# Kernel optimization log

Measured on AMD Instinct MI355X. Metric: run time of the kernel, lower is better.

The kernel has to match this reference:

```python
import jax, jax.numpy as jnp
import numpy as np

B, N, INC, H, W = 1, 6, 256, 56, 100
DD, CC = 41, 64                         # depth bins (4..45 step 1), cam feat channels
NX, NY, NZ = 33, 33, 2                  # BEV grid from pc_range=[-50,-50,-5,50,50,3], grid=3
CZ = CC * NZ                            # 128 channels into bevencode
DXV = jnp.array([3.0, 3.0, 3.0], jnp.float32)
BXV = jnp.array([-48.5, -48.5, -3.5], jnp.float32)


def _frustum():
    ds = jnp.arange(4.0, 45.0, 1.0)                      # (41,)
    xs = jnp.linspace(0.0, 1599.0, W)
    ys = jnp.linspace(0.0, 899.0, H)
    d = jnp.broadcast_to(ds[:, None, None], (DD, H, W))
    xg = jnp.broadcast_to(xs[None, None, :], (DD, H, W))
    yg = jnp.broadcast_to(ys[None, :, None], (DD, H, W))
    return jnp.stack([xg, yg, d], -1)                    # (D,H,W,3)


def _conv(x, w):
    return jax.lax.conv_general_dilated(x, w, (1, 1), 'SAME',
                                        dimension_numbers=('NCHW', 'OIHW', 'NCHW'))


def _bn_relu(x, s, b, m, v):
    inv = s / jnp.sqrt(v + 1e-5)
    return jax.nn.relu(x * inv[None, :, None, None] + (b - m * inv)[None, :, None, None])


def _forward(x, rots, trans, dn_w, dn_b,
             bw1, bn1_s, bn1_b, bn1_m, bn1_v,
             bw2, bn2_s, bn2_b, bn2_m, bn2_v,
             bw3, bn3_s, bn3_b, bn3_m, bn3_v,
             bw4, bn4_s, bn4_b, bn4_m, bn4_v):
    # ---- CamEncode: 1x1 depthnet -> softmax depth dist + context features ----
    xf = x.reshape(B * N, INC, H, W)
    y = _conv(xf, dn_w) + dn_b[None, :, None, None]
    depth = jax.nn.softmax(y[:, :DD], axis=1).reshape(B, N, DD, H, W)
    feat = y[:, DD:DD + CC].reshape(B, N, CC, H, W)
    # ---- get_geometry: (u*d, v*d, d) -> ego frame ----
    fr = _frustum()                                                     # (D,H,W,3)
    pts = jnp.concatenate([fr[..., :2] * fr[..., 2:3], fr[..., 2:3]], -1)
    geom = jnp.einsum('bnij,dhwj->bndhwi', rots, pts) + trans[:, :, None, None, None, :]
    # ---- voxel indices (torch .long() truncates toward zero) ----
    coor = ((geom - (BXV - DXV / 2.0)) / DXV).astype(jnp.int32)         # (B,N,D,H,W,3)
    cx, cy, cz = coor[..., 0], coor[..., 1], coor[..., 2]
    kept = (cx >= 0) & (cx < NX) & (cy >= 0) & (cy < NY) & (cz >= 0) & (cz < NZ)
    bidx = jnp.arange(B, dtype=jnp.int32)[:, None, None, None, None]
    ranks = ((bidx * NZ + cz) * NY + cy) * NX + cx                      # bev rank per point
    nvox = B * NZ * NY * NX
    seg = jnp.where(kept, ranks, nvox).reshape(-1)                      # drop bucket = nvox
    # ---- lift: depth-weighted outer product, splat: segment-sum by voxel ----
    vol = depth[..., None] * feat.transpose(0, 1, 3, 4, 2)[:, :, None]  # (B,N,D,H,W,C)
    bev = jax.ops.segment_sum(vol.reshape(-1, CC), seg, num_segments=nvox + 1)[:nvox]
    bev = bev.reshape(B, NZ, NY, NX, CC).transpose(0, 4, 1, 2, 3).reshape(B, CZ, NY, NX)
    h = _bn_relu(_conv(bev, bw1), bn1_s, bn1_b, bn1_m, bn1_v)
    h = _bn_relu(_conv(h, bw2), bn2_s, bn2_b, bn2_m, bn2_v)
    h = _bn_relu(_conv(h, bw3), bn3_s, bn3_b, bn3_m, bn3_v)
    h = _bn_relu(_conv(h, bw4), bn4_s, bn4_b, bn4_m, bn4_v)
    return h                                                            # (B,256,33,33)


def setup_inputs() -> dict:
    key = jax.random.key(0)
    ks = jax.random.split(key, 16)
    x = jax.random.normal(ks[0], (B, N, INC, H, W), jnp.float32)
    # rots = small rotation perturbation composed with intrinsics inverse
    kinv = jnp.array([[1.0 / 800.0, 0.0, -1.0], [0.0, 1.0 / 800.0, -0.5625], [0.0, 0.0, 1.0]], jnp.float32)
    R = jnp.eye(3, dtype=jnp.float32) + 0.05 * jax.random.normal(ks[1], (B, N, 3, 3), jnp.float32)
    rots = jnp.einsum('bnij,jk->bnik', R, kinv)
    trans = 2.0 * jax.random.normal(ks[2], (B, N, 3), jnp.float32)

    def w(k, o, i, kh, kw):
        return jax.random.normal(k, (o, i, kh, kw), jnp.float32) * (2.0 / (i * kh * kw)) ** 0.5

    def bn(k, c):
        k1, k2, k3, k4 = jax.random.split(k, 4)
        return (1.0 + 0.1 * jax.random.normal(k1, (c,), jnp.float32),
                0.1 * jax.random.normal(k2, (c,), jnp.float32),
                0.1 * jax.random.normal(k3, (c,), jnp.float32),
                jax.random.uniform(k4, (c,), jnp.float32, 0.5, 1.5))
    bn1 = bn(ks[7], CZ); bn2 = bn(ks[8], 512); bn3 = bn(ks[9], 512); bn4 = bn(ks[10], 256)
    return dict(
        x=x, rots=rots, trans=trans,
        dn_w=w(ks[3], DD + CC, INC, 1, 1), dn_b=jnp.zeros((DD + CC,), jnp.float32),
        bw1=w(ks[4], CZ, CZ, 3, 3),
        bn1_s=bn1[0], bn1_b=bn1[1], bn1_m=bn1[2], bn1_v=bn1[3],
        bw2=w(ks[5], 512, CZ, 3, 3),
        bn2_s=bn2[0], bn2_b=bn2[1], bn2_m=bn2[2], bn2_v=bn2[3],
        bw3=w(ks[6], 512, 512, 3, 3),
        bn3_s=bn3[0], bn3_b=bn3[1], bn3_m=bn3[2], bn3_v=bn3[3],
        bw4=w(ks[11], 256, 512, 3, 3),
        bn4_s=bn4[0], bn4_b=bn4[1], bn4_m=bn4[2], bn4_v=bn4[3])


def reference(x, rots, trans, dn_w, dn_b,
              bw1, bn1_s, bn1_b, bn1_m, bn1_v,
              bw2, bn2_s, bn2_b, bn2_m, bn2_v,
              bw3, bn3_s, bn3_b, bn3_m, bn3_v,
              bw4, bn4_s, bn4_b, bn4_m, bn4_v):
    return _forward(x, rots, trans, dn_w, dn_b,
                    bw1, bn1_s, bn1_b, bn1_m, bn1_v,
                    bw2, bn2_s, bn2_b, bn2_m, bn2_v,
                    bw3, bn3_s, bn3_b, bn3_m, bn3_v,
                    bw4, bn4_s, bn4_b, bn4_m, bn4_v)
```

## Files before the change

### kernel.cpp

```cpp
#include <hip/hip_runtime.h>
#include <math.h>

#define NCAM  6
#define INC   256
#define HH    56
#define WW    100
#define HW    5600
#define NPIX  33600
#define DDEP  41
#define CFEAT 64
#define NCH   105
#define NXG   33
#define NYG   33
#define NZG   2
#define NVOX  2178
#define PADW  35
#define PADHW 1225
#define NPIXO 1089

typedef short bf16x8 __attribute__((ext_vector_type(8)));
typedef float f32x4  __attribute__((ext_vector_type(4)));

#define Y_OFF    0
#define Y_SZ     (NCAM * NCH * HW)
#define WDH_OFF  (Y_OFF + Y_SZ)
#define WDL_OFF  (WDH_OFF + 16384)
#define W1H_OFF  (WDL_OFF + 16384)
#define W1L_OFF  (W1H_OFF + 73728)
#define W2H_OFF  (W1L_OFF + 73728)
#define W2L_OFF  (W2H_OFF + 294912)
#define W3H_OFF  (W2L_OFF + 294912)
#define W3L_OFF  (W3H_OFF + 1179648)
#define W4H_OFF  (W3L_OFF + 1179648)
#define W4L_OFF  (W4H_OFF + 589824)
#define BEV_OFF  (W4L_OFF + 589824)
#define BEV_SZ   (NVOX * CFEAT)
#define A1_OFF   (BEV_OFF + BEV_SZ)
#define A2_OFF   (A1_OFF + 313600)
#define A3_OFF   (A2_OFF + 313600)
#define P_OFF    (A3_OFF + 313600)
#define P_SZ     4460544
#define WS_END   (P_OFF + P_SZ)

#define BEV_N4   (BEV_SZ / 4)

__device__ __forceinline__ unsigned short f2bf_rn(float f) {
    unsigned u = __builtin_bit_cast(unsigned, f);
    unsigned r = (u + 0x7FFFu + ((u >> 16) & 1u)) >> 16;
    return (unsigned short)r;
}
__device__ __forceinline__ void split_bf(float f, unsigned short& h, unsigned short& l) {
    h = f2bf_rn(f);
    float hf = __builtin_bit_cast(float, (unsigned)h << 16);
    l = f2bf_rn(f - hf);
}
__device__ __forceinline__ void split_bf_trunc(float f, short& h, short& l) {
    unsigned u = __builtin_bit_cast(unsigned, f);
    h = (short)(u >> 16);
    float hf = __builtin_bit_cast(float, u & 0xFFFF0000u);
    float r = f - hf;
    l = (short)(__builtin_bit_cast(unsigned, r) >> 16);
}

template<int COUT, int CIN>
__device__ __forceinline__ void wprep_conv_t(const float* __restrict__ wgt,
                                             unsigned short* __restrict__ wh,
                                             unsigned short* __restrict__ wl,
                                             int i)
{
    constexpr int NCHK = CIN >> 5;
    constexpr int NCOG = COUT >> 4;
    int jj = i & 7, lane = (i >> 3) & 63;
    int r  = i >> 9;
    int chk = r % NCHK; r /= NCHK;
    int cog = r % NCOG; int dydx = r / NCOG;
    int co = cog * 16 + (lane & 15);
    int ci = chk * 32 + (lane >> 4) * 8 + jj;
    float w = wgt[((size_t)co * CIN + ci) * 9 + dydx];
    unsigned short h, l; split_bf(w, h, l);
    wh[i] = h; wl[i] = l;
}

__global__ __launch_bounds__(256) void k_prep(const float* __restrict__ dnw,
                                              const float* __restrict__ bw1,
                                              const float* __restrict__ bw2,
                                              const float* __restrict__ bw3,
                                              const float* __restrict__ bw4,
                                              unsigned short* __restrict__ wdh,
                                              unsigned short* __restrict__ wdl,
                                              unsigned short* __restrict__ w1h,
                                              unsigned short* __restrict__ w1l,
                                              unsigned short* __restrict__ w2h,
                                              unsigned short* __restrict__ w2l,
                                              unsigned short* __restrict__ w3h,
                                              unsigned short* __restrict__ w3l,
                                              unsigned short* __restrict__ w4h,
                                              unsigned short* __restrict__ w4l,
                                              uint4* __restrict__ bev4)
{
    int i = blockIdx.x * 256 + threadIdx.x;
    if (i < BEV_N4) { bev4[i] = make_uint4(0u, 0u, 0u, 0u); return; }
    i -= BEV_N4;
    if (i < 32768) {
        int jj = i & 7, lane = (i >> 3) & 63, chk = (i >> 9) & 7, ct = i >> 12;
        int co = ct * 16 + (lane & 15);
        int ci = chk * 32 + (lane >> 4) * 8 + jj;
        float w = (co < NCH) ? dnw[co * 256 + ci] : 0.f;
        unsigned short h, l; split_bf(w, h, l);
        wdh[i] = h; wdl[i] = l;
        return;
    }
    i -= 32768;
    if (i < 147456)  { wprep_conv_t<128, 128>(bw1, w1h, w1l, i); return; }
    i -= 147456;
    if (i < 589824)  { wprep_conv_t<512, 128>(bw2, w2h, w2l, i); return; }
    i -= 589824;
    if (i < 2359296) { wprep_conv_t<512, 512>(bw3, w3h, w3l, i); return; }
    i -= 2359296;
    if (i < 1179648) { wprep_conv_t<256, 512>(bw4, w4h, w4l, i); return; }
}
#define PREP_TOTAL (BEV_N4 + 32768 + 147456 + 589824 + 2359296 + 1179648)

__global__ __launch_bounds__(256) void k_depthnet_fused(const float* __restrict__ x,
                                                        const unsigned short* __restrict__ wdh,
                                                        const unsigned short* __restrict__ wdl,
                                                        const float* __restrict__ dnb,
                                                        float* __restrict__ y)
{
    const int t  = threadIdx.x;
    const int w  = t >> 6;
    const int l  = t & 63;
    const int lp = l & 15;
    const int q  = l >> 4;
    const int n   = blockIdx.y;
    const int ct0 = blockIdx.z * 4;
    const int px  = blockIdx.x * 64 + w * 16 + lp;
    const bool pok = px < HW;
    const float* xl = x + (size_t)n * INC * HW + (pok ? px : 0);

    f32x4 acc[4];
#pragma unroll
    for (int ct = 0; ct < 4; ++ct) acc[ct] = (f32x4){0.f, 0.f, 0.f, 0.f};

#pragma unroll 2
    for (int ci0 = 0; ci0 < INC; ci0 += 32) {
        float bv[8];
#pragma unroll
        for (int jj = 0; jj < 8; ++jj)
            bv[jj] = xl[(size_t)(ci0 + q * 8 + jj) * HW];
        bf16x8 Bh, Bl;
#pragma unroll
        for (int jj = 0; jj < 8; ++jj) {
            short h, lo; split_bf_trunc(pok ? bv[jj] : 0.f, h, lo);
            Bh[jj] = h; Bl[jj] = lo;
        }
#pragma unroll
        for (int ct = 0; ct < 4; ++ct) {
            const size_t ab = (size_t)(((ct0 + ct) * 8 + (ci0 >> 5)) * 64 + l) * 8;
            bf16x8 Ah = *(const bf16x8*)&wdh[ab];
            bf16x8 Al = *(const bf16x8*)&wdl[ab];
            acc[ct] = __builtin_amdgcn_mfma_f32_16x16x32_bf16(Ah, Bh, acc[ct], 0, 0, 0);
            acc[ct] = __builtin_amdgcn_mfma_f32_16x16x32_bf16(Ah, Bl, acc[ct], 0, 0, 0);
            acc[ct] = __builtin_amdgcn_mfma_f32_16x16x32_bf16(Al, Bh, acc[ct], 0, 0, 0);
        }
    }

    float v[4][4];
#pragma unroll
    for (int ct = 0; ct < 4; ++ct)
#pragma unroll
        for (int j = 0; j < 4; ++j) {
            int co = (ct0 + ct) * 16 + q * 4 + j;
            v[ct][j] = acc[ct][j] + ((co < NCH) ? dnb[co] : 0.f);
        }

    if (ct0 == 0) {
        float m = -3.4e38f;
#pragma unroll
        for (int ct = 0; ct < 4; ++ct)
#pragma unroll
            for (int j = 0; j < 4; ++j) {
                int co = ct * 16 + q * 4 + j;
                if (co < DDEP) m = fmaxf(m, v[ct][j]);
            }
        m = fmaxf(m, __shfl_xor(m, 16));
        m = fmaxf(m, __shfl_xor(m, 32));
        float e[4][4];
        float s = 0.f;
#pragma unroll
        for (int ct = 0; ct < 4; ++ct)
#pragma unroll
            for (int j = 0; j < 4; ++j) {
                int co = ct * 16 + q * 4 + j;
                e[ct][j] = (co < DDEP) ? expf(v[ct][j] - m) : 0.f;
                s += e[ct][j];
            }
        s += __shfl_xor(s, 16);
        s += __shfl_xor(s, 32);
#pragma unroll
        for (int ct = 0; ct < 4; ++ct)
#pragma unroll
            for (int j = 0; j < 4; ++j) {
                int co = ct * 16 + q * 4 + j;
                if (co < DDEP) v[ct][j] = e[ct][j] / s;
            }
    }

    if (pok) {
#pragma unroll
        for (int ct = 0; ct < 4; ++ct)
#pragma unroll
            for (int j = 0; j < 4; ++j) {
                int co = (ct0 + ct) * 16 + q * 4 + j;
                if (co < NCH)
                    y[((size_t)n * NCH + co) * HW + px] = v[ct][j];
            }
    }
}

__global__ __launch_bounds__(256) void k_splat2(const float* __restrict__ y,
                                                const float* __restrict__ rots,
                                                const float* __restrict__ trans,
                                                float* __restrict__ bev)
{
    __shared__ int vox[32 * DDEP];
    const int t  = threadIdx.x;
    const int p0 = blockIdx.x * 32;

    for (int k = t; k < 32 * DDEP; k += 256) {
        int pl = k / DDEP, d = k - pl * DDEP;
        int p = p0 + pl;
        int vx = -1;
        {
            int n = p / HW, hw = p - n * HW;
            int wi = hw % WW, hi = hw / WW;
            const float su = 1599.0f / 99.0f;
            const float sv = 899.0f / 55.0f;
            float u = __fmul_rn((float)wi, su);
            float v = __fmul_rn((float)hi, sv);
            const float* r = rots + n * 9;
            const float* tr = trans + n * 3;
            float dd  = 4.0f + (float)d;
            float pxv = __fmul_rn(u, dd);
            float pyv = __fmul_rn(v, dd);
            float gx = __fadd_rn(__fadd_rn(__fadd_rn(__fmul_rn(r[0], pxv), __fmul_rn(r[1], pyv)), __fmul_rn(r[2], dd)), tr[0]);
            float gy = __fadd_rn(__fadd_rn(__fadd_rn(__fmul_rn(r[3], pxv), __fmul_rn(r[4], pyv)), __fmul_rn(r[5], dd)), tr[1]);
            float gz = __fadd_rn(__fadd_rn(__fadd_rn(__fmul_rn(r[6], pxv), __fmul_rn(r[7], pyv)), __fmul_rn(r[8], dd)), tr[2]);
            int cx = (int)__fdiv_rn(__fadd_rn(gx, 50.0f), 3.0f);
            int cy = (int)__fdiv_rn(__fadd_rn(gy, 50.0f), 3.0f);
            int cz = (int)__fdiv_rn(__fadd_rn(gz, 5.0f), 3.0f);
            if (cx >= 0 && cx < NXG && cy >= 0 && cy < NYG && cz >= 0 && cz < NZG)
                vx = (cz * NYG + cy) * NXG + cx;
        }
        vox[k] = vx;
    }
    __syncthreads();

    const int g  = t >> 5;
    const int pl = t & 31;
    const int p  = p0 + pl;
    int n = p / HW, hw = p - n * HW;
    const float* dbase = y + (size_t)n * NCH * HW + hw;
    const float* fbase = dbase + (size_t)DDEP * HW;
    float f[8];
#pragma unroll
    for (int j = 0; j < 8; ++j) f[j] = fbase[(size_t)(g * 8 + j) * HW];

    float a[8];
#pragma unroll
    for (int j = 0; j < 8; ++j) a[j] = 0.f;
    int cur = -1;
    for (int d = 0; d < DDEP; ++d) {
        int vx = vox[pl * DDEP + d];
        if (vx != cur) {
            if (cur >= 0) {
                float* vp = bev + (size_t)cur * CFEAT + g * 8;
#pragma unroll
                for (int j = 0; j < 8; ++j) atomicAdd(vp + j, a[j]);
            }
            cur = vx;
#pragma unroll
            for (int j = 0; j < 8; ++j) a[j] = 0.f;
        }
        if (vx >= 0) {
            float dval = dbase[(size_t)d * HW];
#pragma unroll
            for (int j = 0; j < 8; ++j) a[j] += __fmul_rn(dval, f[j]);
        }
    }
    if (cur >= 0) {
        float* vp = bev + (size_t)cur * CFEAT + g * 8;
#pragma unroll
        for (int j = 0; j < 8; ++j) atomicAdd(vp + j, a[j]);
    }
}

template<int CIN, int COUT, int SL, int BEVIN>
__global__ __launch_bounds__(256) void k_conv_mfma(const void* __restrict__ actv,
                                                   const unsigned short* __restrict__ wh,
                                                   const unsigned short* __restrict__ wl,
                                                   float* __restrict__ P)
{
    constexpr int CI_PER = CIN / SL;
    constexpr int CHUNKS = CI_PER / 32;
    constexpr int NSLOT  = CHUNKS * 4;
    constexpr int SMASK  = NSLOT - 1;
    constexpr int ROW    = NSLOT * 8;
    constexpr int NCOB = COUT / 64;
    constexpr int G    = NCOB * SL;
    constexpr int GX   = G / 8;
    constexpr int POSN = 140;
    __shared__ unsigned short bs[POSN * ROW];
    const unsigned short* act = (const unsigned short*)actv;
    const float* bevf = (const float*)actv;
    const int t  = threadIdx.x;
    const int w  = t >> 6;
    const int l  = t & 63;
    const int lp = l & 15;
    const int q  = l >> 4;

    const int bid   = blockIdx.x;
    const int xcd   = bid & 7;
    const int slot  = bid >> 3;
    const int ytile = slot % 17;
    const int gon   = slot / 17;
    const int group = xcd * GX + gon;
    const int cobi  = group % NCOB;
    const int sl    = group / NCOB;

    const int y0  = ytile * 2;
    const int cob = cobi * 64 + w * 16;
    const int ci_base = sl * CI_PER;

    int  pos0[5];
    bool vld[5];
#pragma unroll
    for (int ct = 0; ct < 5; ++ct) {
        int tp = ct * 16 + lp;
        int r = tp / 33, c = tp - r * 33;
        bool v = (tp < 66) && (y0 + r < 33);
        vld[ct]  = v;
        pos0[ct] = v ? (r * 35 + c) : 0;
    }

    for (int i = t; i < POSN * NSLOT; i += 256) {
        int pos = i / NSLOT, s = i - pos * NSLOT;
        int gpos = y0 * 35 + pos;
        int sp = s ^ (pos & SMASK);
        uint4 val = make_uint4(0u, 0u, 0u, 0u);
        if (gpos < PADHW) {
            if constexpr (BEVIN) {
                int gy = gpos / 35, gx = gpos - gy * 35;
                if (gy >= 1 && gy <= 33 && gx >= 1 && gx <= 33) {
                    int vx = (gy - 1) * 33 + (gx - 1);
                    int c0 = (ci_base + s * 8) >> 1;
                    float4 v0 = *(const float4*)&bevf[(size_t)vx * 64 + c0];
                    float4 v1 = *(const float4*)&bevf[(size_t)(NPIXO + vx) * 64 + c0];
                    unsigned short o[8] = { f2bf_rn(v0.x), f2bf_rn(v1.x),
                                            f2bf_rn(v0.y), f2bf_rn(v1.y),
                                            f2bf_rn(v0.z), f2bf_rn(v1.z),
                                            f2bf_rn(v0.w), f2bf_rn(v1.w) };
                    val = *(const uint4*)o;
                }
            } else {
                val = *(const uint4*)&act[(size_t)gpos * CIN + ci_base + s * 8];
            }
        }
        *(uint4*)&bs[pos * ROW + sp * 8] = val;
    }
    __syncthreads();

    f32x4 acc[5];
#pragma unroll
    for (int ct = 0; ct < 5; ++ct) acc[ct] = (f32x4){0.f, 0.f, 0.f, 0.f};

#pragma unroll 3
    for (int dydx = 0; dydx < 9; ++dydx) {
        int dy = dydx / 3, dx = dydx - dy * 3;
        int off = dy * 35 + dx;
        bf16x8 Ah[CHUNKS], Al[CHUNKS];
#pragma unroll
        for (int c = 0; c < CHUNKS; ++c) {
            const size_t abase = (size_t)(((dydx * (COUT >> 4) + (cob >> 4)) * (CIN >> 5)
                                           + (ci_base >> 5) + c) * 64 + l) * 8;
            Ah[c] = *(const bf16x8*)&wh[abase];
            Al[c] = *(const bf16x8*)&wl[abase];
        }
#pragma unroll
        for (int ct = 0; ct < 5; ++ct) {
            int pos = pos0[ct] + off;
#pragma unroll
            for (int c = 0; c < CHUNKS; ++c) {
                int sph = (c * 4 + q) ^ (pos & SMASK);
                bf16x8 B = *(const bf16x8*)&bs[pos * ROW + sph * 8];
                acc[ct] = __builtin_amdgcn_mfma_f32_16x16x32_bf16(Ah[c], B, acc[ct], 0, 0, 0);
                acc[ct] = __builtin_amdgcn_mfma_f32_16x16x32_bf16(Al[c], B, acc[ct], 0, 0, 0);
            }
        }
    }

#pragma unroll
    for (int ct = 0; ct < 5; ++ct) {
        if (!vld[ct]) continue;
        int gp = y0 * 33 + ct * 16 + lp;
        float* dst = P + ((size_t)sl * NPIXO + gp) * COUT + cob + q * 4;
        *(f32x4*)dst = acc[ct];
    }
}

template<int SL, int COUT, int FINAL>
__global__ __launch_bounds__(256) void k_finish(const float* __restrict__ P,
                                                const float* __restrict__ bns,
                                                const float* __restrict__ bnb,
                                                const float* __restrict__ bnm,
                                                const float* __restrict__ bnv,
                                                unsigned short* __restrict__ oact,
                                                float* __restrict__ outf)
{
    int i = blockIdx.x * 256 + threadIdx.x;
    constexpr int NP = FINAL ? NPIXO : PADHW;
    if (i >= COUT * NP) return;
    int co = i % COUT, pos = i / COUT;
    if constexpr (FINAL) {
        float s = 0.f;
#pragma unroll
        for (int sl = 0; sl < SL; ++sl)
            s += P[((size_t)sl * NPIXO + pos) * COUT + co];
        float sc = bns[co] / sqrtf(bnv[co] + 1e-5f);
        float bi = bnb[co] - bnm[co] * sc;
        outf[(size_t)co * NPIXO + pos] = fmaxf(fmaf(s, sc, bi), 0.f);
    } else {
        int py = pos / 35, px2 = pos - py * 35;
        bool inz = (py >= 1) && (py <= 33) && (px2 >= 1) && (px2 <= 33);
        unsigned short ov = 0;
        if (inz) {
            int p = (py - 1) * 33 + (px2 - 1);
            float s = 0.f;
#pragma unroll
            for (int sl = 0; sl < SL; ++sl)
                s += P[((size_t)sl * NPIXO + p) * COUT + co];
            float sc = bns[co] / sqrtf(bnv[co] + 1e-5f);
            float bi = bnb[co] - bnm[co] * sc;
            ov = f2bf_rn(fmaxf(fmaf(s, sc, bi), 0.f));
        }
        oact[(size_t)pos * COUT + co] = ov;
    }
}

extern "C" void kernel_launch(void* const* d_in, const int* in_sizes, int n_in,
                              void* d_out, int out_size, void* d_ws, size_t ws_size,
                              hipStream_t stream)
{
    const float* x     = (const float*)d_in[0];
    const float* rots  = (const float*)d_in[1];
    const float* trans = (const float*)d_in[2];
    const float* dnw   = (const float*)d_in[3];
    const float* dnb   = (const float*)d_in[4];
    const float* bw1   = (const float*)d_in[5];
    const float* bn1s  = (const float*)d_in[6];
    const float* bn1b  = (const float*)d_in[7];
    const float* bn1m  = (const float*)d_in[8];
    const float* bn1v  = (const float*)d_in[9];
    const float* bw2   = (const float*)d_in[10];
    const float* bn2s  = (const float*)d_in[11];
    const float* bn2b  = (const float*)d_in[12];
    const float* bn2m  = (const float*)d_in[13];
    const float* bn2v  = (const float*)d_in[14];
    const float* bw3   = (const float*)d_in[15];
    const float* bn3s  = (const float*)d_in[16];
    const float* bn3b  = (const float*)d_in[17];
    const float* bn3m  = (const float*)d_in[18];
    const float* bn3v  = (const float*)d_in[19];
    const float* bw4   = (const float*)d_in[20];
    const float* bn4s  = (const float*)d_in[21];
    const float* bn4b  = (const float*)d_in[22];
    const float* bn4m  = (const float*)d_in[23];
    const float* bn4v  = (const float*)d_in[24];

    float* ws  = (float*)d_ws;
    float* y   = ws + Y_OFF;
    float* bev = ws + BEV_OFF;
    float* P   = ws + P_OFF;
    unsigned short* wdh = (unsigned short*)(ws + WDH_OFF);
    unsigned short* wdl = (unsigned short*)(ws + WDL_OFF);
    unsigned short* w1h = (unsigned short*)(ws + W1H_OFF);
    unsigned short* w1l = (unsigned short*)(ws + W1L_OFF);
    unsigned short* w2h = (unsigned short*)(ws + W2H_OFF);
    unsigned short* w2l = (unsigned short*)(ws + W2L_OFF);
    unsigned short* w3h = (unsigned short*)(ws + W3H_OFF);
    unsigned short* w3l = (unsigned short*)(ws + W3L_OFF);
    unsigned short* w4h = (unsigned short*)(ws + W4H_OFF);
    unsigned short* w4l = (unsigned short*)(ws + W4L_OFF);
    unsigned short* a1  = (unsigned short*)(ws + A1_OFF);
    unsigned short* a2  = (unsigned short*)(ws + A2_OFF);
    unsigned short* a3  = (unsigned short*)(ws + A3_OFF);
    float* out = (float*)d_out;

    k_prep<<<(PREP_TOTAL + 255) / 256, 256, 0, stream>>>(dnw, bw1, bw2, bw3, bw4,
                                                         wdh, wdl, w1h, w1l, w2h, w2l,
                                                         w3h, w3l, w4h, w4l, (uint4*)bev);
    k_depthnet_fused<<<dim3(88, 6, 2), 256, 0, stream>>>(x, wdh, wdl, dnb, y);
    k_splat2<<<1050, 256, 0, stream>>>(y, rots, trans, bev);

    k_conv_mfma<128, 128, 4, 1><<<136, 256, 0, stream>>>(bev, w1h, w1l, P);
    k_finish<4, 128, 0><<<(128 * PADHW + 255) / 256, 256, 0, stream>>>(P, bn1s, bn1b, bn1m, bn1v, a1, nullptr);
    k_conv_mfma<128, 512, 4, 0><<<544, 256, 0, stream>>>(a1, w2h, w2l, P);
    k_finish<4, 512, 0><<<(512 * PADHW + 255) / 256, 256, 0, stream>>>(P, bn2s, bn2b, bn2m, bn2v, a2, nullptr);
    k_conv_mfma<512, 512, 4, 0><<<544, 256, 0, stream>>>(a2, w3h, w3l, P);
    k_finish<4, 512, 0><<<(512 * PADHW + 255) / 256, 256, 0, stream>>>(P, bn3s, bn3b, bn3m, bn3v, a3, nullptr);
    k_conv_mfma<512, 256, 8, 0><<<544, 256, 0, stream>>>(a3, w4h, w4l, P);
    k_finish<8, 256, 1><<<(256 * NPIXO + 255) / 256, 256, 0, stream>>>(P, bn4s, bn4b, bn4m, bn4v, nullptr, out);
}
```

Before: 120.5 us.

## Fuse split-K reduction and BN+ReLU into next conv's input staging

Removes the three intermediate k_finish kernels. Each following conv now reads the previous layer's split-K partial sums directly while staging its input, sums them, applies the BN scale/bias and ReLU, and rounds to bf16 in the load path. Two ping-pong partial buffers replace the single P buffer and the bf16 activation buffers. This saves three launches and one write/read round trip of the activations. In exchange, each conv block re-reads fp32 partials, four slices per element, and halo rows are re-reduced by neighbouring tiles, so input global traffic per conv goes up.

```diff
diff --git a/kernel.cpp b/kernel.cpp
--- a/kernel.cpp
+++ b/kernel.cpp
@@ -35,12 +35,10 @@
 #define W4L_OFF  (W4H_OFF + 589824)
 #define BEV_OFF  (W4L_OFF + 589824)
 #define BEV_SZ   (NVOX * CFEAT)
-#define A1_OFF   (BEV_OFF + BEV_SZ)
-#define A2_OFF   (A1_OFF + 313600)
-#define A3_OFF   (A2_OFF + 313600)
-#define P_OFF    (A3_OFF + 313600)
-#define P_SZ     4460544
-#define WS_END   (P_OFF + P_SZ)
+#define PA_OFF   (BEV_OFF + BEV_SZ)
+#define PBUF_SZ  2230272
+#define PB_OFF   (PA_OFF + PBUF_SZ)
+#define WS_END   (PB_OFF + PBUF_SZ)
 
 #define BEV_N4   (BEV_SZ / 4)
 
@@ -295,8 +293,12 @@
     }
 }
 
-template<int CIN, int COUT, int SL, int BEVIN>
-__global__ __launch_bounds__(256) void k_conv_mfma(const void* __restrict__ actv,
+template<int CIN, int COUT, int SL, int SLP, int MODE>
+__global__ __launch_bounds__(256) void k_conv_mfma(const void* __restrict__ inv,
+                                                   const float* __restrict__ bns,
+                                                   const float* __restrict__ bnb,
+                                                   const float* __restrict__ bnm,
+                                                   const float* __restrict__ bnv,
                                                    const unsigned short* __restrict__ wh,
                                                    const unsigned short* __restrict__ wl,
                                                    float* __restrict__ P)
@@ -311,8 +313,9 @@
     constexpr int GX   = G / 8;
     constexpr int POSN = 140;
     __shared__ unsigned short bs[POSN * ROW];
-    const unsigned short* act = (const unsigned short*)actv;
-    const float* bevf = (const float*)actv;
+    __shared__ float scb[MODE == 0 ? CI_PER * 2 : 2];
+    const float* Pin  = (const float*)inv;
+    const float* bevf = (const float*)inv;
     const int t  = threadIdx.x;
     const int w  = t >> 6;
     const int l  = t & 63;
@@ -343,27 +346,56 @@
         pos0[ct] = v ? (r * 35 + c) : 0;
     }
 
+    if constexpr (MODE == 0) {
+        for (int c = t; c < CI_PER; c += 256) {
+            int ci = ci_base + c;
+            float sc = bns[ci] / sqrtf(bnv[ci] + 1e-5f);
+            scb[c * 2]     = sc;
+            scb[c * 2 + 1] = bnb[ci] - bnm[ci] * sc;
+        }
+        __syncthreads();
+    }
+
     for (int i = t; i < POSN * NSLOT; i += 256) {
         int pos = i / NSLOT, s = i - pos * NSLOT;
         int gpos = y0 * 35 + pos;
         int sp = s ^ (pos & SMASK);
         uint4 val = make_uint4(0u, 0u, 0u, 0u);
         if (gpos < PADHW) {
-            if constexpr (BEVIN) {
-                int gy = gpos / 35, gx = gpos - gy * 35;
-                if (gy >= 1 && gy <= 33 && gx >= 1 && gx <= 33) {
-                    int vx = (gy - 1) * 33 + (gx - 1);
+            int gy = gpos / 35, gx = gpos - gy * 35;
+            bool inz = (gy >= 1) && (gy <= 33) && (gx >= 1) && (gx <= 33);
+            if (inz) {
+                int p = (gy - 1) * 33 + (gx - 1);
+                if constexpr (MODE == 1) {
                     int c0 = (ci_base + s * 8) >> 1;
-                    float4 v0 = *(const float4*)&bevf[(size_t)vx * 64 + c0];
-                    float4 v1 = *(const float4*)&bevf[(size_t)(NPIXO + vx) * 64 + c0];
+                    float4 v0 = *(const float4*)&bevf[(size_t)p * 64 + c0];
+                    float4 v1 = *(const float4*)&bevf[(size_t)(NPIXO + p) * 64 + c0];
                     unsigned short o[8] = { f2bf_rn(v0.x), f2bf_rn(v1.x),
                                             f2bf_rn(v0.y), f2bf_rn(v1.y),
                                             f2bf_rn(v0.z), f2bf_rn(v1.z),
                                             f2bf_rn(v0.w), f2bf_rn(v1.w) };
                     val = *(const uint4*)o;
+                } else {
+                    float sum[8];
+#pragma unroll
+                    for (int j = 0; j < 8; ++j) sum[j] = 0.f;
+#pragma unroll
+                    for (int ps = 0; ps < SLP; ++ps) {
+                        const float* src = &Pin[((size_t)ps * NPIXO + p) * CIN + ci_base + s * 8];
+                        float4 u0 = *(const float4*)src;
+                        float4 u1 = *(const float4*)(src + 4);
+                        sum[0] += u0.x; sum[1] += u0.y; sum[2] += u0.z; sum[3] += u0.w;
+                        sum[4] += u1.x; sum[5] += u1.y; sum[6] += u1.z; sum[7] += u1.w;
+                    }
+                    unsigned short o[8];
+#pragma unroll
+                    for (int j = 0; j < 8; ++j) {
+                        int cl = s * 8 + j;
+                        float rv = fmaxf(fmaf(sum[j], scb[cl * 2], scb[cl * 2 + 1]), 0.f);
+                        o[j] = f2bf_rn(rv);
+                    }
+                    val = *(const uint4*)o;
                 }
-            } else {
-                val = *(const uint4*)&act[(size_t)gpos * CIN + ci_base + s * 8];
             }
         }
         *(uint4*)&bs[pos * ROW + sp * 8] = val;
@@ -408,43 +440,24 @@
     }
 }
 
-template<int SL, int COUT, int FINAL>
-__global__ __launch_bounds__(256) void k_finish(const float* __restrict__ P,
-                                                const float* __restrict__ bns,
-                                                const float* __restrict__ bnb,
-                                                const float* __restrict__ bnm,
-                                                const float* __restrict__ bnv,
-                                                unsigned short* __restrict__ oact,
-                                                float* __restrict__ outf)
+template<int SL, int COUT>
+__global__ __launch_bounds__(256) void k_finish_final(const float* __restrict__ P,
+                                                      const float* __restrict__ bns,
+                                                      const float* __restrict__ bnb,
+                                                      const float* __restrict__ bnm,
+                                                      const float* __restrict__ bnv,
+                                                      float* __restrict__ outf)
 {
     int i = blockIdx.x * 256 + threadIdx.x;
-    constexpr int NP = FINAL ? NPIXO : PADHW;
-    if (i >= COUT * NP) return;
+    if (i >= COUT * NPIXO) return;
     int co = i % COUT, pos = i / COUT;
-    if constexpr (FINAL) {
-        float s = 0.f;
-#pragma unroll
-        for (int sl = 0; sl < SL; ++sl)
-            s += P[((size_t)sl * NPIXO + pos) * COUT + co];
-        float sc = bns[co] / sqrtf(bnv[co] + 1e-5f);
-        float bi = bnb[co] - bnm[co] * sc;
-        outf[(size_t)co * NPIXO + pos] = fmaxf(fmaf(s, sc, bi), 0.f);
-    } else {
-        int py = pos / 35, px2 = pos - py * 35;
-        bool inz = (py >= 1) && (py <= 33) && (px2 >= 1) && (px2 <= 33);
-        unsigned short ov = 0;
-        if (inz) {
-            int p = (py - 1) * 33 + (px2 - 1);
-            float s = 0.f;
-#pragma unroll
-            for (int sl = 0; sl < SL; ++sl)
-                s += P[((size_t)sl * NPIXO + p) * COUT + co];
-            float sc = bns[co] / sqrtf(bnv[co] + 1e-5f);
-            float bi = bnb[co] - bnm[co] * sc;
-            ov = f2bf_rn(fmaxf(fmaf(s, sc, bi), 0.f));
-        }
-        oact[(size_t)pos * COUT + co] = ov;
-    }
+    float s = 0.f;
+#pragma unroll
+    for (int sl = 0; sl < SL; ++sl)
+        s += P[((size_t)sl * NPIXO + pos) * COUT + co];
+    float sc = bns[co] / sqrtf(bnv[co] + 1e-5f);
+    float bi = bnb[co] - bnm[co] * sc;
+    outf[(size_t)co * NPIXO + pos] = fmaxf(fmaf(s, sc, bi), 0.f);
 }
 
 extern "C" void kernel_launch(void* const* d_in, const int* in_sizes, int n_in,
@@ -480,7 +493,8 @@
     float* ws  = (float*)d_ws;
     float* y   = ws + Y_OFF;
     float* bev = ws + BEV_OFF;
-    float* P   = ws + P_OFF;
+    float* PA  = ws + PA_OFF;
+    float* PB  = ws + PB_OFF;
     unsigned short* wdh = (unsigned short*)(ws + WDH_OFF);
     unsigned short* wdl = (unsigned short*)(ws + WDL_OFF);
     unsigned short* w1h = (unsigned short*)(ws + W1H_OFF);
@@ -491,9 +505,6 @@
     unsigned short* w3l = (unsigned short*)(ws + W3L_OFF);
     unsigned short* w4h = (unsigned short*)(ws + W4H_OFF);
     unsigned short* w4l = (unsigned short*)(ws + W4L_OFF);
-    unsigned short* a1  = (unsigned short*)(ws + A1_OFF);
-    unsigned short* a2  = (unsigned short*)(ws + A2_OFF);
-    unsigned short* a3  = (unsigned short*)(ws + A3_OFF);
     float* out = (float*)d_out;
 
     k_prep<<<(PREP_TOTAL + 255) / 256, 256, 0, stream>>>(dnw, bw1, bw2, bw3, bw4,
@@ -502,12 +513,13 @@
     k_depthnet_fused<<<dim3(88, 6, 2), 256, 0, stream>>>(x, wdh, wdl, dnb, y);
     k_splat2<<<1050, 256, 0, stream>>>(y, rots, trans, bev);
 
-    k_conv_mfma<128, 128, 4, 1><<<136, 256, 0, stream>>>(bev, w1h, w1l, P);
-    k_finish<4, 128, 0><<<(128 * PADHW + 255) / 256, 256, 0, stream>>>(P, bn1s, bn1b, bn1m, bn1v, a1, nullptr);
-    k_conv_mfma<128, 512, 4, 0><<<544, 256, 0, stream>>>(a1, w2h, w2l, P);
-    k_finish<4, 512, 0><<<(512 * PADHW + 255) / 256, 256, 0, stream>>>(P, bn2s, bn2b, bn2m, bn2v, a2, nullptr);
-    k_conv_mfma<512, 512, 4, 0><<<544, 256, 0, stream>>>(a2, w3h, w3l, P);
-    k_finish<4, 512, 0><<<(512 * PADHW + 255) / 256, 256, 0, stream>>>(P, bn3s, bn3b, bn3m, bn3v, a3, nullptr);
-    k_conv_mfma<512, 256, 8, 0><<<544, 256, 0, stream>>>(a3, w4h, w4l, P);
-    k_finish<8, 256, 1><<<(256 * NPIXO + 255) / 256, 256, 0, stream>>>(P, bn4s, bn4b, bn4m, bn4v, nullptr, out);
-}
+    k_conv_mfma<128, 128, 4, 1, 1><<<136, 256, 0, stream>>>(bev, nullptr, nullptr, nullptr, nullptr,
+                                                            w1h, w1l, PA);
+    k_conv_mfma<128, 512, 4, 4, 0><<<544, 256, 0, stream>>>(PA, bn1s, bn1b, bn1m, bn1v,
+                                                            w2h, w2l, PB);
+    k_conv_mfma<512, 512, 4, 4, 0><<<544, 256, 0, stream>>>(PB, bn2s, bn2b, bn2m, bn2v,
+                                                            w3h, w3l, PA);
+    k_conv_mfma<512, 256, 8, 4, 0><<<544, 256, 0, stream>>>(PA, bn3s, bn3b, bn3m, bn3v,
+                                                            w4h, w4l, PB);
+    k_finish_final<8, 256><<<(256 * NPIXO + 255) / 256, 256, 0, stream>>>(PB, bn4s, bn4b, bn4m, bn4v, out);
+}
```

Measured after the change: 125.5 us. 1.04x slower.
